# Optimization experiments

Measured on AMD Instinct MI355X. Metric: run time of the kernel, lower is better.

Reference implementation:

```python
import jax, jax.numpy as jnp
import numpy as np

# Config matching the torch module
NUM_HEADS = 12
NUM_FRAMES = 8
NUM_THEADS = 2
DIM = 768
HEAD_DIM = DIM // NUM_HEADS
SCALE = HEAD_DIM ** -0.5
ADAPTER_SCALE = 1.0


def setup_inputs() -> dict:
    key = jax.random.key(0)
    ks = jax.random.split(key, 6)
    BT, N, C = 64, 197, DIM  # 8 videos * 8 frames, 197 tokens
    H = int(C * 0.25)  # adapter hidden = 192
    std = 0.02
    return {
        "x": jax.random.normal(ks[0], (BT, N, C), jnp.float32),
        "a_w1": jax.random.normal(ks[1], (C, H), jnp.float32) * std,
        "a_b1": jnp.zeros((H,), jnp.float32),
        "a_w2": jax.random.normal(ks[2], (H, C), jnp.float32) * std,
        "a_b2": jnp.zeros((C,), jnp.float32),
        "qkv_w": jax.random.normal(ks[3], (C, 3 * C), jnp.float32) * std,
        "qkv_b": jnp.zeros((3 * C,), jnp.float32),
        "proj_w": jax.random.normal(ks[4], (C, C), jnp.float32) * std,
        "proj_b": jnp.zeros((C,), jnp.float32),
    }


def head_reallocation(x):
    # x: [BT, H, N, hd] -> temporal shift of first NUM_THEADS heads (from past frame)
    # and next NUM_THEADS heads (from future frame).
    bt, h, n, d = x.shape
    feat = x.reshape(bt // NUM_FRAMES, NUM_FRAMES, h, n, d)
    out = feat
    out = out.at[:, 1:, :NUM_THEADS].set(feat[:, :-1, :NUM_THEADS])
    out = out.at[:, :-1, NUM_THEADS:2 * NUM_THEADS].set(feat[:, 1:, NUM_THEADS:2 * NUM_THEADS])
    return out.reshape(bt, h, n, d)


def reference(x, a_w1, a_b1, a_w2, a_b2, qkv_w, qkv_b, proj_w, proj_b):
    B, N, C = x.shape
    # shared input adapter (skip connection, scale=1)
    xs = (x @ a_w1 + a_b1) @ a_w2 + a_b2
    x = x + xs * ADAPTER_SCALE
    # fused qkv projection -> [3, B, H, N, hd]
    qkv = (x @ qkv_w + qkv_b).reshape(B, N, 3, NUM_HEADS, HEAD_DIM)
    qkv = jnp.transpose(qkv, (2, 0, 3, 1, 4))
    q, k, v = qkv[0], qkv[1], qkv[2]
    k = head_reallocation(k)
    v = head_reallocation(v)
    attn = jnp.einsum("bhqd,bhkd->bhqk", q, k) * SCALE
    attn = jax.nn.softmax(attn, axis=-1)
    out = jnp.einsum("bhqk,bhkd->bhqd", attn, v)
    out = jnp.transpose(out, (0, 2, 1, 3)).reshape(B, N, C)
    return out @ proj_w + proj_b
```

## Files before the change

### kernel.cpp

```cpp
#include <hip/hip_runtime.h>
#include <hip/hip_bf16.h>

typedef unsigned short u16;
typedef __attribute__((ext_vector_type(8))) short bf16x8;
typedef __attribute__((ext_vector_type(8))) unsigned short u16x8;
typedef __attribute__((ext_vector_type(4))) float f32x4;

#define NBT 64
#define SEQ 197
#define CDIM 768
#define NH 12
#define HD 64
#define MVALID (NBT * SEQ)
#define MPAD 12672
#define HADP 192
#define HPAD 256
#define QKVSZ (NBT * NH * SEQ * HD)

__device__ __forceinline__ u16 f2b(float f) {
    __hip_bfloat16 h = __float2bfloat16(f);
    return __builtin_bit_cast(u16, h);
}

#define GLL16(gp, lp) __builtin_amdgcn_global_load_lds( \
    (__attribute__((address_space(1))) void*)(gp),      \
    (__attribute__((address_space(3))) void*)(lp), 16, 0, 0)

__global__ __launch_bounds__(256) void cast_x_kernel(const float* __restrict__ x, u16* __restrict__ xb) {
    long i = ((long)blockIdx.x * 256 + threadIdx.x) * 8;
    u16x8 r;
    if (i < (long)MVALID * CDIM) {
        const float4* p = (const float4*)(x + i);
        float4 a = p[0], b = p[1];
        r[0] = f2b(a.x); r[1] = f2b(a.y); r[2] = f2b(a.z); r[3] = f2b(a.w);
        r[4] = f2b(b.x); r[5] = f2b(b.y); r[6] = f2b(b.z); r[7] = f2b(b.w);
    } else {
#pragma unroll
        for (int j = 0; j < 8; ++j) r[j] = 0;
    }
    *(u16x8*)(xb + i) = r;
}

__global__ __launch_bounds__(256) void transpose_cast_kernel(
    const float* __restrict__ in, u16* __restrict__ out, int K, int N, int KP) {
    __shared__ float tile[64][65];
    int k0 = blockIdx.x * 64;
    int n0 = blockIdx.y * 64;
    int c  = threadIdx.x & 63;
    int r0 = threadIdx.x >> 6;
#pragma unroll
    for (int rr = r0; rr < 64; rr += 4) {
        int k = k0 + rr, n = n0 + c;
        tile[rr][c] = (k < K && n < N) ? in[(long)k * N + n] : 0.f;
    }
    __syncthreads();
#pragma unroll
    for (int rr = r0; rr < 64; rr += 4) {
        out[(long)(n0 + rr) * KP + k0 + c] = f2b(tile[c][rr]);
    }
}

template <int MODE, int NB>
__device__ __forceinline__ void gemm_body(
    const u16* __restrict__ A, const u16* __restrict__ Bt,
    const float* __restrict__ bias, const float* __restrict__ resid,
    u16* __restrict__ ob, float* __restrict__ of, int K) {
    __shared__ __align__(16) u16 As[128 * 64];
    __shared__ __align__(16) u16 Bs[128 * 64];
    const int tid  = threadIdx.x;
    const int lane = tid & 63;
    const int w    = tid >> 6;
    const int wm   = w >> 1, wn = w & 1;

    const int nwg  = (int)gridDim.x;
    const int bid  = (int)blockIdx.x;
    const int q    = nwg >> 3, r = nwg & 7;
    const int xcd  = bid & 7;
    const int lid  = bid >> 3;
    const int wgid = (xcd < r ? xcd * (q + 1) : r * (q + 1) + (xcd - r) * q) + lid;
    const long m0  = (long)(wgid / NB) * 128;
    const long n0  = (long)(wgid % NB) * 128;

    const int rA = lane >> 3;
    const int cA = (lane & 7) * 8;

    const u16* ga[4];
    const u16* gb[4];
#pragma unroll
    for (int ii = 0; ii < 4; ++ii) {
        int i = w * 4 + ii;
        ga[ii] = A  + (m0 + i * 8 + rA) * K + cA;
        gb[ii] = Bt + (n0 + i * 8 + rA) * K + cA;
    }

    int aoff[4], boff[4];
#pragma unroll
    for (int t = 0; t < 4; ++t) {
        aoff[t] = (wm * 64 + t * 16 + (lane & 15)) * 64 + (lane >> 4) * 8;
        boff[t] = (wn * 64 + t * 16 + (lane & 15)) * 64 + (lane >> 4) * 8;
    }

    f32x4 acc[4][4] = {};
    const int kSteps = K >> 6;
    for (int kt = 0; kt < kSteps; ++kt) {
#pragma unroll
        for (int ii = 0; ii < 4; ++ii) {
            int i = w * 4 + ii;
            GLL16(ga[ii] + kt * 64, &As[i * 512]);
            GLL16(gb[ii] + kt * 64, &Bs[i * 512]);
        }
        __syncthreads();
#pragma unroll
        for (int kc = 0; kc < 2; ++kc) {
            bf16x8 af[4], bg[4];
#pragma unroll
            for (int t = 0; t < 4; ++t) af[t] = *(const bf16x8*)&As[aoff[t] + kc * 32];
#pragma unroll
            for (int t = 0; t < 4; ++t) bg[t] = *(const bf16x8*)&Bs[boff[t] + kc * 32];
#pragma unroll
            for (int mi = 0; mi < 4; ++mi)
#pragma unroll
                for (int ni = 0; ni < 4; ++ni)
                    acc[mi][ni] = __builtin_amdgcn_mfma_f32_16x16x32_bf16(af[mi], bg[ni], acc[mi][ni], 0, 0, 0);
        }
        __syncthreads();
    }

    const int rb = (lane >> 4) * 4;
    const int cl = lane & 15;
#pragma unroll
    for (int mi = 0; mi < 4; ++mi) {
#pragma unroll
        for (int rr = 0; rr < 4; ++rr) {
            long m = m0 + wm * 64 + mi * 16 + rb + rr;
#pragma unroll
            for (int ni = 0; ni < 4; ++ni) {
                long n = n0 + wn * 64 + ni * 16 + cl;
                float v = acc[mi][ni][rr];
                if constexpr (MODE == 0) {
                    float bv = (n < HADP) ? bias[n] : 0.f;
                    ob[m * HPAD + n] = f2b(v + bv);
                } else if constexpr (MODE == 1) {
                    float val = 0.f;
                    if (m < MVALID) val = v + bias[n] + resid[m * CDIM + n];
                    ob[m * CDIM + n] = f2b(val);
                } else if constexpr (MODE == 2) {
                    if (m < MVALID) {
                        int mm = (int)m;
                        int bb = mm / SEQ;
                        int t  = mm - bb * SEQ;
                        int nn = (int)n;
                        int which = nn / CDIM;
                        int c  = nn - which * CDIM;
                        int hh = c >> 6, d = c & 63;
                        ob[(long)which * QKVSZ + ((long)(bb * NH + hh) * SEQ + t) * HD + d] = f2b(v + bias[nn]);
                    }
                } else {
                    if (m < MVALID) of[m * CDIM + n] = v + bias[n];
                }
            }
        }
    }
}

__global__ __launch_bounds__(256, 4) void gemm_a1(
    const u16* __restrict__ A, const u16* __restrict__ Bt, const float* __restrict__ bias,
    u16* __restrict__ ob, int K) {
    gemm_body<0, 2>(A, Bt, bias, nullptr, ob, nullptr, K);
}
__global__ __launch_bounds__(256, 4) void gemm_a2(
    const u16* __restrict__ A, const u16* __restrict__ Bt, const float* __restrict__ bias,
    const float* __restrict__ resid, u16* __restrict__ ob, int K) {
    gemm_body<1, 6>(A, Bt, bias, resid, ob, nullptr, K);
}
__global__ __launch_bounds__(256, 4) void gemm_qkv(
    const u16* __restrict__ A, const u16* __restrict__ Bt, const float* __restrict__ bias,
    u16* __restrict__ ob, int K) {
    gemm_body<2, 18>(A, Bt, bias, nullptr, ob, nullptr, K);
}
__global__ __launch_bounds__(256, 4) void gemm_proj(
    const u16* __restrict__ A, const u16* __restrict__ Bt, const float* __restrict__ bias,
    float* __restrict__ of, int K) {
    gemm_body<3, 6>(A, Bt, bias, nullptr, nullptr, of, K);
}

__global__ __launch_bounds__(256, 2) void attn_kernel(
    const u16* __restrict__ qb, const u16* __restrict__ kb, const u16* __restrict__ vb,
    u16* __restrict__ aout) {
    __shared__ __align__(16) u16 Vt[64 * 232];
    __shared__ __align__(16) u16 P[4][16 * 232];
    const int bid = blockIdx.x;
    const int b = bid / NH;
    const int h = bid - b * NH;
    const int f = b & 7;
    int fs = (h < 2) ? (f > 0 ? f - 1 : 0) : ((h < 4) ? (f < 7 ? f + 1 : 7) : f);
    const int bsrc = (b & ~7) + fs;
    const u16* Qp = qb + (long)(b    * NH + h) * SEQ * HD;
    const u16* Kp = kb + (long)(bsrc * NH + h) * SEQ * HD;
    const u16* Vp = vb + (long)(bsrc * NH + h) * SEQ * HD;

    const int tid  = threadIdx.x;
    const int lane = tid & 63;
    const int w    = tid >> 6;
    const int cl   = lane & 15;
    const int lg   = lane >> 4;

    {
        unsigned int* z1 = (unsigned int*)Vt;
        for (int i = tid; i < 64 * 232 / 2; i += 256) z1[i] = 0;
        unsigned int* z2 = (unsigned int*)&P[0][0];
        for (int i = tid; i < 4 * 16 * 232 / 2; i += 256) z2[i] = 0;
    }
    __syncthreads();
    for (int g = tid; g < SEQ * HD / 8; g += 256) {
        int t  = g >> 3;
        int d0 = (g & 7) * 8;
        u16x8 v = *(const u16x8*)(Vp + g * 8);
#pragma unroll
        for (int j = 0; j < 8; ++j) Vt[(d0 + j) * 232 + t] = v[j];
    }
    __syncthreads();

    const f32x4 vzero = {0.f, 0.f, 0.f, 0.f};
    u16* Pw = &P[w][0];
    for (int rt = w; rt < 13; rt += 4) {
        int qrow = rt * 16 + cl; if (qrow > SEQ - 1) qrow = SEQ - 1;
        bf16x8 qf0 = *(const bf16x8*)(Qp + qrow * HD + lg * 8);
        bf16x8 qf1 = *(const bf16x8*)(Qp + qrow * HD + 32 + lg * 8);
        f32x4 s[13];
#pragma unroll
        for (int ct = 0; ct < 13; ++ct) s[ct] = vzero;
#pragma unroll
        for (int ct = 0; ct < 13; ++ct) {
            int krow = ct * 16 + cl; if (krow > SEQ - 1) krow = SEQ - 1;
            bf16x8 kf0 = *(const bf16x8*)(Kp + krow * HD + lg * 8);
            bf16x8 kf1 = *(const bf16x8*)(Kp + krow * HD + 32 + lg * 8);
            s[ct] = __builtin_amdgcn_mfma_f32_16x16x32_bf16(qf0, kf0, s[ct], 0, 0, 0);
            s[ct] = __builtin_amdgcn_mfma_f32_16x16x32_bf16(qf1, kf1, s[ct], 0, 0, 0);
        }
        float rm[4] = {-1e30f, -1e30f, -1e30f, -1e30f};
#pragma unroll
        for (int ct = 0; ct < 13; ++ct) {
            bool valid = (ct * 16 + cl) <= SEQ - 1;
#pragma unroll
            for (int r = 0; r < 4; ++r) {
                float v = valid ? s[ct][r] * 0.125f : -1e30f;
                s[ct][r] = v;
                rm[r] = fmaxf(rm[r], v);
            }
        }
#pragma unroll
        for (int off = 1; off <= 8; off <<= 1)
#pragma unroll
            for (int r = 0; r < 4; ++r) rm[r] = fmaxf(rm[r], __shfl_xor(rm[r], off));
        float rs[4] = {0.f, 0.f, 0.f, 0.f};
#pragma unroll
        for (int ct = 0; ct < 13; ++ct)
#pragma unroll
            for (int r = 0; r < 4; ++r) {
                float p = __expf(s[ct][r] - rm[r]);
                s[ct][r] = p;
                rs[r] += p;
            }
#pragma unroll
        for (int off = 1; off <= 8; off <<= 1)
#pragma unroll
            for (int r = 0; r < 4; ++r) rs[r] += __shfl_xor(rs[r], off);
        float inv[4];
#pragma unroll
        for (int r = 0; r < 4; ++r) inv[r] = 1.f / rs[r];

        asm volatile("s_waitcnt lgkmcnt(0)" ::: "memory");
#pragma unroll
        for (int ct = 0; ct < 13; ++ct)
#pragma unroll
            for (int r = 0; r < 4; ++r)
                Pw[(lg * 4 + r) * 232 + ct * 16 + cl] = f2b(s[ct][r] * inv[r]);
        asm volatile("s_waitcnt lgkmcnt(0)" ::: "memory");

        bf16x8 pf[7];
#pragma unroll
        for (int ks = 0; ks < 7; ++ks)
            pf[ks] = *(const bf16x8*)(Pw + cl * 232 + ks * 32 + lg * 8);
#pragma unroll
        for (int dt = 0; dt < 4; ++dt) {
            f32x4 o = vzero;
#pragma unroll
            for (int ks = 0; ks < 7; ++ks) {
                bf16x8 vf = *(const bf16x8*)(&Vt[(dt * 16 + cl) * 232 + ks * 32 + lg * 8]);
                o = __builtin_amdgcn_mfma_f32_16x16x32_bf16(pf[ks], vf, o, 0, 0, 0);
            }
#pragma unroll
            for (int r = 0; r < 4; ++r) {
                int m = rt * 16 + lg * 4 + r;
                if (m < SEQ)
                    aout[(long)(b * SEQ + m) * CDIM + h * HD + dt * 16 + cl] = f2b(o[r]);
            }
        }
    }
}

extern "C" void kernel_launch(void* const* d_in, const int* in_sizes, int n_in,
                              void* d_out, int out_size, void* d_ws, size_t ws_size,
                              hipStream_t stream) {
    const float* x      = (const float*)d_in[0];
    const float* a_w1   = (const float*)d_in[1];
    const float* a_b1   = (const float*)d_in[2];
    const float* a_w2   = (const float*)d_in[3];
    const float* a_b2   = (const float*)d_in[4];
    const float* qkv_w  = (const float*)d_in[5];
    const float* qkv_b  = (const float*)d_in[6];
    const float* proj_w = (const float*)d_in[7];
    const float* proj_b = (const float*)d_in[8];
    float* out = (float*)d_out;
    char* ws = (char*)d_ws;

    u16* xb   = (u16*)(ws + 0);
    u16* xa   = (u16*)(ws + 19464192);
    u16* hbuf = (u16*)(ws + 38928384);
    u16* w1t  = (u16*)(ws + 45416448);
    u16* w2t  = (u16*)(ws + 45809664);
    u16* qwt  = (u16*)(ws + 46202880);
    u16* pwt  = (u16*)(ws + 49741824);
    u16* qkv  = (u16*)(ws + 50921472);
    u16* aout = xb;

    cast_x_kernel<<<4752, 256, 0, stream>>>(x, xb);
    transpose_cast_kernel<<<dim3(12, 4),  256, 0, stream>>>(a_w1,   w1t, 768, 192,  768);
    transpose_cast_kernel<<<dim3(4, 12),  256, 0, stream>>>(a_w2,   w2t, 192, 768,  256);
    transpose_cast_kernel<<<dim3(12, 36), 256, 0, stream>>>(qkv_w,  qwt, 768, 2304, 768);
    transpose_cast_kernel<<<dim3(12, 12), 256, 0, stream>>>(proj_w, pwt, 768, 768,  768);

    gemm_a1  <<<99 * 2,  256, 0, stream>>>(xb,   w1t, a_b1,  hbuf, 768);
    gemm_a2  <<<99 * 6,  256, 0, stream>>>(hbuf, w2t, a_b2,  x, xa, 256);
    gemm_qkv <<<99 * 18, 256, 0, stream>>>(xa,   qwt, qkv_b, qkv,   768);
    attn_kernel<<<NBT * NH, 256, 0, stream>>>(qkv, qkv + QKVSZ, qkv + 2 * (long)QKVSZ, aout);
    gemm_proj<<<99 * 6,  256, 0, stream>>>(aout, pwt, proj_b, out,  768);
}
```

Before: 311.0 us.

## Use 256x256 tile 8-wave pipelined GEMM for QKV and output projections

Replaces the 128x128 GEMMs for the QKV and output projections with a new 512-thread kernel using 256x256 tiles and a 4-stage LDS ring. Global-to-LDS loads are issued two steps ahead and split between the two halves of each K-step's MFMA work, with barriers and setprio used to interleave loads and compute. The M padding grows to 12800 so it is a multiple of 256, which shifts workspace offsets and the launch grids of the other kernels. Larger tiles cut redundant operand traffic, but they leave far fewer workgroups (450 and 150), which can underfill the GPU, especially for the projection GEMM.

```diff
diff --git a/kernel.cpp b/kernel.cpp
--- a/kernel.cpp
+++ b/kernel.cpp
@@ -12,7 +12,7 @@
 #define NH 12
 #define HD 64
 #define MVALID (NBT * SEQ)
-#define MPAD 12672
+#define MPAD 12800
 #define HADP 192
 #define HPAD 256
 #define QKVSZ (NBT * NH * SEQ * HD)
@@ -57,6 +57,33 @@
 #pragma unroll
     for (int rr = r0; rr < 64; rr += 4) {
         out[(long)(n0 + rr) * KP + k0 + c] = f2b(tile[c][rr]);
+    }
+}
+
+template <int MODE>
+__device__ __forceinline__ void epi_store(long m, long n, float v,
+    const float* __restrict__ bias, const float* __restrict__ resid,
+    u16* __restrict__ ob, float* __restrict__ of) {
+    if constexpr (MODE == 0) {
+        float bv = (n < HADP) ? bias[n] : 0.f;
+        ob[m * HPAD + n] = f2b(v + bv);
+    } else if constexpr (MODE == 1) {
+        float val = 0.f;
+        if (m < MVALID) val = v + bias[n] + resid[m * CDIM + n];
+        ob[m * CDIM + n] = f2b(val);
+    } else if constexpr (MODE == 2) {
+        if (m < MVALID) {
+            int mm = (int)m;
+            int bb = mm / SEQ;
+            int t  = mm - bb * SEQ;
+            int nn = (int)n;
+            int which = nn / CDIM;
+            int c  = nn - which * CDIM;
+            int hh = c >> 6, d = c & 63;
+            ob[(long)which * QKVSZ + ((long)(bb * NH + hh) * SEQ + t) * HD + d] = f2b(v + bias[nn]);
+        }
+    } else {
+        if (m < MVALID) of[m * CDIM + n] = v + bias[n];
     }
 }
 
@@ -129,38 +156,14 @@
     const int rb = (lane >> 4) * 4;
     const int cl = lane & 15;
 #pragma unroll
-    for (int mi = 0; mi < 4; ++mi) {
+    for (int mi = 0; mi < 4; ++mi)
 #pragma unroll
         for (int rr = 0; rr < 4; ++rr) {
             long m = m0 + wm * 64 + mi * 16 + rb + rr;
 #pragma unroll
-            for (int ni = 0; ni < 4; ++ni) {
-                long n = n0 + wn * 64 + ni * 16 + cl;
-                float v = acc[mi][ni][rr];
-                if constexpr (MODE == 0) {
-                    float bv = (n < HADP) ? bias[n] : 0.f;
-                    ob[m * HPAD + n] = f2b(v + bv);
-                } else if constexpr (MODE == 1) {
-                    float val = 0.f;
-                    if (m < MVALID) val = v + bias[n] + resid[m * CDIM + n];
-                    ob[m * CDIM + n] = f2b(val);
-                } else if constexpr (MODE == 2) {
-                    if (m < MVALID) {
-                        int mm = (int)m;
-                        int bb = mm / SEQ;
-                        int t  = mm - bb * SEQ;
-                        int nn = (int)n;
-                        int which = nn / CDIM;
-                        int c  = nn - which * CDIM;
-                        int hh = c >> 6, d = c & 63;
-                        ob[(long)which * QKVSZ + ((long)(bb * NH + hh) * SEQ + t) * HD + d] = f2b(v + bias[nn]);
-                    }
-                } else {
-                    if (m < MVALID) of[m * CDIM + n] = v + bias[n];
-                }
-            }
-        }
-    }
+            for (int ni = 0; ni < 4; ++ni)
+                epi_store<MODE>(m, n0 + wn * 64 + ni * 16 + cl, acc[mi][ni][rr], bias, resid, ob, of);
+        }
 }
 
 __global__ __launch_bounds__(256, 4) void gemm_a1(
@@ -173,15 +176,143 @@
     const float* __restrict__ resid, u16* __restrict__ ob, int K) {
     gemm_body<1, 6>(A, Bt, bias, resid, ob, nullptr, K);
 }
-__global__ __launch_bounds__(256, 4) void gemm_qkv(
-    const u16* __restrict__ A, const u16* __restrict__ Bt, const float* __restrict__ bias,
-    u16* __restrict__ ob, int K) {
-    gemm_body<2, 18>(A, Bt, bias, nullptr, ob, nullptr, K);
-}
-__global__ __launch_bounds__(256, 4) void gemm_proj(
-    const u16* __restrict__ A, const u16* __restrict__ Bt, const float* __restrict__ bias,
-    float* __restrict__ of, int K) {
-    gemm_body<3, 6>(A, Bt, bias, nullptr, nullptr, of, K);
+
+template <int MODE, int NB, int NT>
+__global__ __launch_bounds__(512, 2) void gemm8p(
+    const u16* __restrict__ A, const u16* __restrict__ Bt,
+    const float* __restrict__ bias,
+    u16* __restrict__ ob, float* __restrict__ of, int K) {
+    __shared__ __align__(16) u16 As[4][256 * 32];
+    __shared__ __align__(16) u16 Bs[4][256 * 32];
+    const int tid  = threadIdx.x;
+    const int lane = tid & 63;
+    const int w    = tid >> 6;
+    const int wm   = w >> 2;
+    const int wn   = w & 3;
+
+    const int nwg  = (int)gridDim.x;
+    const int bid  = (int)blockIdx.x;
+    const int q    = nwg >> 3, r = nwg & 7;
+    const int xcd  = bid & 7;
+    const int lid  = bid >> 3;
+    const int wgid = (xcd < r ? xcd * (q + 1) : r * (q + 1) + (xcd - r) * q) + lid;
+    const long m0  = (long)(wgid / NB) * 256;
+    const long n0  = (long)(wgid % NB) * 256;
+
+    const int cA    = w * 2;
+    const int srow  = lane >> 2;
+    const int scol  = 8 * ((lane & 3) ^ ((lane >> 2) & 3));
+    const u16* gA0 = A  + (m0 + cA * 16 + srow) * K + scol;
+    const u16* gA1 = gA0 + 16 * K;
+    const u16* gB0 = Bt + (n0 + cA * 16 + srow) * K + scol;
+    const u16* gB1 = gB0 + 16 * K;
+    u16* lA = &As[0][cA * 512];
+    u16* lB = &Bs[0][cA * 512];
+
+    const int xcol = ((lane >> 4) * 8) ^ ((lane & 3) << 3);
+    const int aob  = (wm * 128 + (lane & 15)) * 32 + xcol;
+    const int bob  = (wn * 64  + (lane & 15)) * 32 + xcol;
+
+    f32x4 acc[8][4] = {};
+
+    GLL16(gA0,          lA);            GLL16(gA1,          lA + 512);
+    GLL16(gB0,          lB);            GLL16(gB1,          lB + 512);
+    GLL16(gA0 + 32,     lA + 8192);     GLL16(gA1 + 32,     lA + 8192 + 512);
+    GLL16(gB0 + 32,     lB + 8192);     GLL16(gB1 + 32,     lB + 8192 + 512);
+    asm volatile("s_waitcnt vmcnt(4)" ::: "memory");
+    __builtin_amdgcn_s_barrier();
+
+    for (int j = 0; j < NT; ++j) {
+        const int sj = j & 3;
+        const u16* as = &As[sj][0];
+        const u16* bs = &Bs[sj][0];
+        const int s2 = (j + 2) & 3;
+        const int k2 = (j + 2) * 32;
+        bf16x8 af0, af1, af2, af3, bg0, bg1, bg2, bg3;
+
+        af0 = *(const bf16x8*)(as + aob);
+        af1 = *(const bf16x8*)(as + aob + 512);
+        af2 = *(const bf16x8*)(as + aob + 1024);
+        af3 = *(const bf16x8*)(as + aob + 1536);
+        bg0 = *(const bf16x8*)(bs + bob);
+        bg1 = *(const bf16x8*)(bs + bob + 512);
+        bg2 = *(const bf16x8*)(bs + bob + 1024);
+        bg3 = *(const bf16x8*)(bs + bob + 1536);
+        if (j + 2 < NT) {
+            GLL16(gA0 + k2, lA + s2 * 8192);
+            GLL16(gA1 + k2, lA + s2 * 8192 + 512);
+        }
+        __builtin_amdgcn_s_barrier();
+        asm volatile("s_waitcnt lgkmcnt(0)" ::: "memory");
+        __builtin_amdgcn_sched_barrier(0);
+        __builtin_amdgcn_s_setprio(1);
+        acc[0][0] = __builtin_amdgcn_mfma_f32_16x16x32_bf16(af0, bg0, acc[0][0], 0, 0, 0);
+        acc[0][1] = __builtin_amdgcn_mfma_f32_16x16x32_bf16(af0, bg1, acc[0][1], 0, 0, 0);
+        acc[0][2] = __builtin_amdgcn_mfma_f32_16x16x32_bf16(af0, bg2, acc[0][2], 0, 0, 0);
+        acc[0][3] = __builtin_amdgcn_mfma_f32_16x16x32_bf16(af0, bg3, acc[0][3], 0, 0, 0);
+        acc[1][0] = __builtin_amdgcn_mfma_f32_16x16x32_bf16(af1, bg0, acc[1][0], 0, 0, 0);
+        acc[1][1] = __builtin_amdgcn_mfma_f32_16x16x32_bf16(af1, bg1, acc[1][1], 0, 0, 0);
+        acc[1][2] = __builtin_amdgcn_mfma_f32_16x16x32_bf16(af1, bg2, acc[1][2], 0, 0, 0);
+        acc[1][3] = __builtin_amdgcn_mfma_f32_16x16x32_bf16(af1, bg3, acc[1][3], 0, 0, 0);
+        acc[2][0] = __builtin_amdgcn_mfma_f32_16x16x32_bf16(af2, bg0, acc[2][0], 0, 0, 0);
+        acc[2][1] = __builtin_amdgcn_mfma_f32_16x16x32_bf16(af2, bg1, acc[2][1], 0, 0, 0);
+        acc[2][2] = __builtin_amdgcn_mfma_f32_16x16x32_bf16(af2, bg2, acc[2][2], 0, 0, 0);
+        acc[2][3] = __builtin_amdgcn_mfma_f32_16x16x32_bf16(af2, bg3, acc[2][3], 0, 0, 0);
+        acc[3][0] = __builtin_amdgcn_mfma_f32_16x16x32_bf16(af3, bg0, acc[3][0], 0, 0, 0);
+        acc[3][1] = __builtin_amdgcn_mfma_f32_16x16x32_bf16(af3, bg1, acc[3][1], 0, 0, 0);
+        acc[3][2] = __builtin_amdgcn_mfma_f32_16x16x32_bf16(af3, bg2, acc[3][2], 0, 0, 0);
+        acc[3][3] = __builtin_amdgcn_mfma_f32_16x16x32_bf16(af3, bg3, acc[3][3], 0, 0, 0);
+        __builtin_amdgcn_s_setprio(0);
+        __builtin_amdgcn_s_barrier();
+
+        af0 = *(const bf16x8*)(as + aob + 2048);
+        af1 = *(const bf16x8*)(as + aob + 2560);
+        af2 = *(const bf16x8*)(as + aob + 3072);
+        af3 = *(const bf16x8*)(as + aob + 3584);
+        if (j + 2 < NT) {
+            GLL16(gB0 + k2, lB + s2 * 8192);
+            GLL16(gB1 + k2, lB + s2 * 8192 + 512);
+        }
+        __builtin_amdgcn_s_barrier();
+        asm volatile("s_waitcnt lgkmcnt(0)" ::: "memory");
+        __builtin_amdgcn_sched_barrier(0);
+        __builtin_amdgcn_s_setprio(1);
+        acc[4][0] = __builtin_amdgcn_mfma_f32_16x16x32_bf16(af0, bg0, acc[4][0], 0, 0, 0);
+        acc[4][1] = __builtin_amdgcn_mfma_f32_16x16x32_bf16(af0, bg1, acc[4][1], 0, 0, 0);
+        acc[4][2] = __builtin_amdgcn_mfma_f32_16x16x32_bf16(af0, bg2, acc[4][2], 0, 0, 0);
+        acc[4][3] = __builtin_amdgcn_mfma_f32_16x16x32_bf16(af0, bg3, acc[4][3], 0, 0, 0);
+        acc[5][0] = __builtin_amdgcn_mfma_f32_16x16x32_bf16(af1, bg0, acc[5][0], 0, 0, 0);
+        acc[5][1] = __builtin_amdgcn_mfma_f32_16x16x32_bf16(af1, bg1, acc[5][1], 0, 0, 0);
+        acc[5][2] = __builtin_amdgcn_mfma_f32_16x16x32_bf16(af1, bg2, acc[5][2], 0, 0, 0);
+        acc[5][3] = __builtin_amdgcn_mfma_f32_16x16x32_bf16(af1, bg3, acc[5][3], 0, 0, 0);
+        acc[6][0] = __builtin_amdgcn_mfma_f32_16x16x32_bf16(af2, bg0, acc[6][0], 0, 0, 0);
+        acc[6][1] = __builtin_amdgcn_mfma_f32_16x16x32_bf16(af2, bg1, acc[6][1], 0, 0, 0);
+        acc[6][2] = __builtin_amdgcn_mfma_f32_16x16x32_bf16(af2, bg2, acc[6][2], 0, 0, 0);
+        acc[6][3] = __builtin_amdgcn_mfma_f32_16x16x32_bf16(af2, bg3, acc[6][3], 0, 0, 0);
+        acc[7][0] = __builtin_amdgcn_mfma_f32_16x16x32_bf16(af3, bg0, acc[7][0], 0, 0, 0);
+        acc[7][1] = __builtin_amdgcn_mfma_f32_16x16x32_bf16(af3, bg1, acc[7][1], 0, 0, 0);
+        acc[7][2] = __builtin_amdgcn_mfma_f32_16x16x32_bf16(af3, bg2, acc[7][2], 0, 0, 0);
+        acc[7][3] = __builtin_amdgcn_mfma_f32_16x16x32_bf16(af3, bg3, acc[7][3], 0, 0, 0);
+        __builtin_amdgcn_s_setprio(0);
+        if (j + 2 < NT) {
+            asm volatile("s_waitcnt vmcnt(4)" ::: "memory");
+        } else if (j + 1 < NT) {
+            asm volatile("s_waitcnt vmcnt(0)" ::: "memory");
+        }
+        __builtin_amdgcn_s_barrier();
+    }
+
+    const int rb = (lane >> 4) * 4;
+    const int cl = lane & 15;
+#pragma unroll
+    for (int mi = 0; mi < 8; ++mi)
+#pragma unroll
+        for (int rr = 0; rr < 4; ++rr) {
+            long m = m0 + wm * 128 + mi * 16 + rb + rr;
+#pragma unroll
+            for (int ni = 0; ni < 4; ++ni)
+                epi_store<MODE>(m, n0 + wn * 64 + ni * 16 + cl, acc[mi][ni][rr], bias, nullptr, ob, of);
+        }
 }
 
 __global__ __launch_bounds__(256, 2) void attn_kernel(
@@ -316,24 +447,24 @@
     char* ws = (char*)d_ws;
 
     u16* xb   = (u16*)(ws + 0);
-    u16* xa   = (u16*)(ws + 19464192);
-    u16* hbuf = (u16*)(ws + 38928384);
-    u16* w1t  = (u16*)(ws + 45416448);
-    u16* w2t  = (u16*)(ws + 45809664);
-    u16* qwt  = (u16*)(ws + 46202880);
-    u16* pwt  = (u16*)(ws + 49741824);
-    u16* qkv  = (u16*)(ws + 50921472);
+    u16* xa   = (u16*)(ws + 19660800);
+    u16* hbuf = (u16*)(ws + 39321600);
+    u16* w1t  = (u16*)(ws + 45875200);
+    u16* w2t  = (u16*)(ws + 46268416);
+    u16* qwt  = (u16*)(ws + 46661632);
+    u16* pwt  = (u16*)(ws + 50200576);
+    u16* qkv  = (u16*)(ws + 51380224);
     u16* aout = xb;
 
-    cast_x_kernel<<<4752, 256, 0, stream>>>(x, xb);
+    cast_x_kernel<<<4800, 256, 0, stream>>>(x, xb);
     transpose_cast_kernel<<<dim3(12, 4),  256, 0, stream>>>(a_w1,   w1t, 768, 192,  768);
     transpose_cast_kernel<<<dim3(4, 12),  256, 0, stream>>>(a_w2,   w2t, 192, 768,  256);
     transpose_cast_kernel<<<dim3(12, 36), 256, 0, stream>>>(qkv_w,  qwt, 768, 2304, 768);
     transpose_cast_kernel<<<dim3(12, 12), 256, 0, stream>>>(proj_w, pwt, 768, 768,  768);
 
-    gemm_a1  <<<99 * 2,  256, 0, stream>>>(xb,   w1t, a_b1,  hbuf, 768);
-    gemm_a2  <<<99 * 6,  256, 0, stream>>>(hbuf, w2t, a_b2,  x, xa, 256);
-    gemm_qkv <<<99 * 18, 256, 0, stream>>>(xa,   qwt, qkv_b, qkv,   768);
+    gemm_a1<<<100 * 2, 256, 0, stream>>>(xb,   w1t, a_b1, hbuf, 768);
+    gemm_a2<<<100 * 6, 256, 0, stream>>>(hbuf, w2t, a_b2, x, xa, 256);
+    gemm8p<2, 9, 24><<<50 * 9, 512, 0, stream>>>(xa, qwt, qkv_b, qkv, nullptr, 768);
     attn_kernel<<<NBT * NH, 256, 0, stream>>>(qkv, qkv + QKVSZ, qkv + 2 * (long)QKVSZ, aout);
-    gemm_proj<<<99 * 6,  256, 0, stream>>>(aout, pwt, proj_b, out,  768);
-}
+    gemm8p<3, 3, 24><<<50 * 3, 512, 0, stream>>>(aout, pwt, proj_b, nullptr, out, 768);
+}
```

After: 357.2 us. 1.15x slower.
